# Optimization experiments

Measured on AMD Instinct MI355X. Metric: run time of the kernel, lower is better.

## Reference

```python
import jax, jax.numpy as jnp
import numpy as np

N, E, D, IN_DIM, EDGE_DIM, L = 50000, 800000, 128, 11, 4, 4
G, MID, SPEC = 500, 256, 300  # num graphs, decoder mid width, per-head spectrum dim
MSG_IN = 2 * D + EDGE_DIM + 1  # h_i, h_j, edge_attr, d2


def _lin_init(key, fan_in, shape):
    return jax.random.uniform(key, shape, jnp.float32, -1.0, 1.0) / np.sqrt(fan_in)


def setup_inputs() -> dict:
    key = jax.random.key(0)
    ks = iter(jax.random.split(key, 64))
    inp = {
        'x': jax.random.normal(next(ks), (N, IN_DIM), jnp.float32),
        'pos': jax.random.normal(next(ks), (N, 3), jnp.float32),
        'edge_attr': jax.random.normal(next(ks), (E, EDGE_DIM), jnp.float32),
        'edge_index': jax.random.randint(next(ks), (2, E), 0, N, jnp.int32),
        'batch': jnp.sort(jax.random.randint(next(ks), (N,), 0, G, jnp.int32)),
        # input projection
        'W_in': _lin_init(next(ks), IN_DIM, (IN_DIM, D)),
        'b_in': jnp.zeros((D,), jnp.float32),
        # per-layer message MLP: Linear(2D+de+1 -> D), ReLU, Linear(D -> D)
        'msg_W1': _lin_init(next(ks), MSG_IN, (L, MSG_IN, D)),
        'msg_b1': jnp.zeros((L, D), jnp.float32),
        'msg_W2': _lin_init(next(ks), D, (L, D, D)),
        'msg_b2': jnp.zeros((L, D), jnp.float32),
        # per-layer update MLP: Linear(2D -> D), ReLU, Linear(D -> D)
        'upd_W1': _lin_init(next(ks), 2 * D, (L, 2 * D, D)),
        'upd_b1': jnp.zeros((L, D), jnp.float32),
        'upd_W2': _lin_init(next(ks), D, (L, D, D)),
        'upd_b2': jnp.zeros((L, D), jnp.float32),
        # per-layer LayerNorm
        'ln_g': jnp.ones((L, D), jnp.float32),
        'ln_b': jnp.zeros((L, D), jnp.float32),
        # decoder heads stacked: index 0 = energy, 1 = intensity
        'dec_W1': _lin_init(next(ks), D, (2, D, MID)),
        'dec_b1': jnp.zeros((2, MID), jnp.float32),
        'dec_lng': jnp.ones((2, MID), jnp.float32),
        'dec_lnb': jnp.zeros((2, MID), jnp.float32),
        'dec_W2': _lin_init(next(ks), MID, (2, MID, MID)),
        'dec_b2': jnp.zeros((2, MID), jnp.float32),
        'dec_W3': _lin_init(next(ks), MID, (2, MID, SPEC)),
        'dec_b3': jnp.zeros((2, SPEC), jnp.float32),
    }
    return inp


def _ln(x, g, b, eps=1e-5):
    m = x.mean(-1, keepdims=True)
    v = ((x - m) ** 2).mean(-1, keepdims=True)
    return (x - m) * jax.lax.rsqrt(v + eps) * g + b


def _softplus_beta(x, beta):
    return jax.nn.softplus(beta * x) / beta


def reference(x, pos, edge_attr, edge_index, batch,
              W_in, b_in, msg_W1, msg_b1, msg_W2, msg_b2,
              upd_W1, upd_b1, upd_W2, upd_b2, ln_g, ln_b,
              dec_W1, dec_b1, dec_lng, dec_lnb, dec_W2, dec_b2, dec_W3, dec_b3):
    n = x.shape[0]
    src, dst = edge_index[0], edge_index[1]  # message flows j(src) -> i(dst)
    h = x @ W_in + b_in  # (n, d)
    rel = pos[dst] - pos[src]  # (e, 3)
    d2 = jnp.sum(rel * rel, axis=-1, keepdims=True)  # (e, 1), invariant squared distance
    for l in range(L):
        m_in = jnp.concatenate([h[dst], h[src], edge_attr, d2], axis=-1)  # (e, 2d+de+1)
        m = jax.nn.relu(m_in @ msg_W1[l] + msg_b1[l]) @ msg_W2[l] + msg_b2[l]  # (e, d)
        agg = jax.ops.segment_sum(m, dst, num_segments=n)  # (n, d) sum aggregation
        u_in = jnp.concatenate([h, agg], axis=-1)  # (n, 2d)
        h_upd = jax.nn.relu(u_in @ upd_W1[l] + upd_b1[l]) @ upd_W2[l] + upd_b2[l]
        h = _ln(h + h_upd, ln_g[l], ln_b[l])  # residual + LayerNorm
    # global mean pool per graph
    hs = jax.ops.segment_sum(h, batch, num_segments=G)
    cnt = jax.ops.segment_sum(jnp.ones((n,), h.dtype), batch, num_segments=G)
    hg = hs / jnp.clip(cnt, 1.0)[:, None]  # (G, d)

    def head(i):
        z = _softplus_beta(_ln(hg @ dec_W1[i] + dec_b1[i], dec_lng[i], dec_lnb[i]), 2.0)
        z = _softplus_beta(z @ dec_W2[i] + dec_b2[i], 2.0)  # dropout = identity (eval)
        return _softplus_beta(z @ dec_W3[i] + dec_b3[i], 1.0)

    eng, intensity = head(0), head(1)
    return jnp.concatenate([eng, intensity], axis=-1)  # (G, 2*SPEC)
```

## Files before the change

kernel.cpp:

```cpp
#include <hip/hip_runtime.h>
#include <cstdint>
#include <cstddef>

#define NND 50000
#define NE  800000
#define DD  128
#define NG  500
#define TT  64
#define NHB 50176

typedef __attribute__((ext_vector_type(8))) short short8v;
typedef __attribute__((ext_vector_type(4))) float float4v;

__device__ __forceinline__ short f2bf(float f) {
    unsigned u = __builtin_bit_cast(unsigned, f);
    unsigned r = (u + 0x7FFFu + ((u >> 16) & 1u)) >> 16;
    return (short)r;
}

__global__ __launch_bounds__(256) void inproj_kernel(
    const float* __restrict__ x, const float* __restrict__ W,
    const float* __restrict__ b, float* __restrict__ h)
{
    int t = blockIdx.x * 256 + threadIdx.x;
    int i = t >> 7, d = t & 127;
    if (i >= NND) return;
    const float* xr = x + (size_t)i * 11;
    float acc = b[d];
#pragma unroll
    for (int k = 0; k < 11; ++k) acc += xr[k] * W[k * DD + d];
    h[(size_t)i * DD + d] = acc;
}

__global__ __launch_bounds__(256) void hist_kernel(
    const int* __restrict__ dstI, int* __restrict__ hist)
{
    int e = blockIdx.x * 256 + threadIdx.x;
    if (e >= NE) return;
    atomicAdd(&hist[dstI[e]], 1);
}

__global__ __launch_bounds__(256) void scan1_kernel(
    int* __restrict__ hist, int* __restrict__ bsum)
{
    __shared__ int s[256];
    int tid = threadIdx.x;
    int i = blockIdx.x * 256 + tid;
    int v = hist[i];
    s[tid] = v; __syncthreads();
    for (int off = 1; off < 256; off <<= 1) {
        int tmp = (tid >= off) ? s[tid - off] : 0;
        __syncthreads();
        s[tid] += tmp;
        __syncthreads();
    }
    hist[i] = s[tid] - v;
    if (tid == 255) bsum[blockIdx.x] = s[255];
}

__global__ __launch_bounds__(256) void scan2_kernel(
    const int* __restrict__ bsum, int* __restrict__ bsumx)
{
    __shared__ int s[256];
    int tid = threadIdx.x;
    int v = (tid < 196) ? bsum[tid] : 0;
    s[tid] = v; __syncthreads();
    for (int off = 1; off < 256; off <<= 1) {
        int tmp = (tid >= off) ? s[tid - off] : 0;
        __syncthreads();
        s[tid] += tmp;
        __syncthreads();
    }
    if (tid < 196) bsumx[tid] = s[tid] - v;
}

__global__ __launch_bounds__(256) void scan3_kernel(
    int* __restrict__ hist, const int* __restrict__ bsumx)
{
    int i = blockIdx.x * 256 + threadIdx.x;
    hist[i] += bsumx[blockIdx.x];
}

__global__ __launch_bounds__(256) void scatter_kernel(
    const int* __restrict__ dstI, int* __restrict__ cursor, int* __restrict__ perm)
{
    int e = blockIdx.x * 256 + threadIdx.x;
    if (e >= NE) return;
    int pos = atomicAdd(&cursor[dstI[e]], 1);
    perm[pos] = e;
}

__global__ __launch_bounds__(256) void permapply_kernel(
    const int* __restrict__ perm, const int* __restrict__ srcI, const int* __restrict__ dstI,
    const float* __restrict__ ea,
    int* __restrict__ srcP, int* __restrict__ dstP, float* __restrict__ eaP)
{
    int i = blockIdx.x * 256 + threadIdx.x;
    if (i >= NE) return;
    int e = perm[i];
    srcP[i] = srcI[e];
    dstP[i] = dstI[e];
    ((float4*)eaP)[i] = ((const float4*)ea)[e];
}

__global__ __launch_bounds__(256) void d2p_kernel(
    const float* __restrict__ pos, const int* __restrict__ srcP,
    const int* __restrict__ dstP, float* __restrict__ d2)
{
    int e = blockIdx.x * 256 + threadIdx.x;
    if (e >= NE) return;
    int s = srcP[e], d = dstP[e];
    float dx = pos[d * 3 + 0] - pos[s * 3 + 0];
    float dy = pos[d * 3 + 1] - pos[s * 3 + 1];
    float dz = pos[d * 3 + 2] - pos[s * 3 + 2];
    d2[e] = dx * dx + dy * dy + dz * dz;
}

__global__ __launch_bounds__(256) void d2_kernel(
    const float* __restrict__ pos, const int* __restrict__ srcI,
    const int* __restrict__ dstI, float* __restrict__ d2)
{
    int e = blockIdx.x * 256 + threadIdx.x;
    if (e >= NE) return;
    int s = srcI[e], d = dstI[e];
    float dx = pos[d * 3 + 0] - pos[s * 3 + 0];
    float dy = pos[d * 3 + 1] - pos[s * 3 + 1];
    float dz = pos[d * 3 + 2] - pos[s * 3 + 2];
    d2[e] = dx * dx + dy * dy + dz * dz;
}

__global__ __launch_bounds__(256) void w2prep_kernel(
    const float* __restrict__ W2, short* __restrict__ W2t)
{
    int p = blockIdx.x * 256 + threadIdx.x;
    int n = p >> 7;
    int q = (p & 127) >> 3;
    int j = p & 7;
    int kg = q ^ (n & 7);
    W2t[p] = f2bf(W2[(kg * 8 + j) * DD + n]);
}

__global__ __launch_bounds__(256, 4) void proj_kernel(
    const float* __restrict__ h, const float* __restrict__ W1, float* __restrict__ P)
{
    __shared__ __align__(16) float A[32][TT];
    __shared__ __align__(16) float B[32][DD];
    int i0 = blockIdx.x * TT;
    int mat = blockIdx.y;
    const float* W = W1 + (size_t)mat * 128 * DD;
    float* out = P + (size_t)mat * NND * DD;
    int t = threadIdx.x;
    int tx = t & 15, ty = t >> 4;
    int e = t & 63, q = t >> 6;
    int node = i0 + e; if (node >= NND) node = NND - 1;
    const float* hrow = h + (size_t)node * DD;

    float acc[4][8];
#pragma unroll
    for (int i = 0; i < 4; ++i)
#pragma unroll
        for (int j = 0; j < 8; ++j) acc[i][j] = 0.0f;

    for (int c = 0; c < 4; ++c) {
        __syncthreads();
        float4 v0 = *(const float4*)(hrow + c * 32 + q * 8);
        float4 v1 = *(const float4*)(hrow + c * 32 + q * 8 + 4);
#pragma unroll
        for (int j = 0; j < 4; ++j) A[q * 8 + j][e]     = (&v0.x)[j];
#pragma unroll
        for (int j = 0; j < 4; ++j) A[q * 8 + 4 + j][e] = (&v1.x)[j];
        const float4* srcp = (const float4*)(W + (size_t)(c * 32) * DD);
        float4* dstp = (float4*)&B[0][0];
#pragma unroll
        for (int r = 0; r < 4; ++r) dstp[t + r * 256] = srcp[t + r * 256];
        __syncthreads();
#pragma unroll 4
        for (int k = 0; k < 32; ++k) {
            float4 a  = *(const float4*)&A[k][tx * 4];
            float4 b0 = *(const float4*)&B[k][ty * 8];
            float4 b1 = *(const float4*)&B[k][ty * 8 + 4];
            float av[4] = {a.x, a.y, a.z, a.w};
            float bv[8] = {b0.x, b0.y, b0.z, b0.w, b1.x, b1.y, b1.z, b1.w};
#pragma unroll
            for (int i = 0; i < 4; ++i)
#pragma unroll
                for (int j = 0; j < 8; ++j) acc[i][j] += av[i] * bv[j];
        }
    }
#pragma unroll
    for (int i = 0; i < 4; ++i) {
        int r = i0 + tx * 4 + i;
        if (r < NND) {
            float4 o0 = {acc[i][0], acc[i][1], acc[i][2], acc[i][3]};
            float4 o1 = {acc[i][4], acc[i][5], acc[i][6], acc[i][7]};
            *(float4*)(out + (size_t)r * DD + ty * 8)     = o0;
            *(float4*)(out + (size_t)r * DD + ty * 8 + 4) = o1;
        }
    }
}

__global__ __launch_bounds__(256, 3) void msgm_kernel(
    const float* __restrict__ P, const int* __restrict__ srcP, const int* __restrict__ dstP,
    const float* __restrict__ eaP, const float* __restrict__ d2,
    const float* __restrict__ W1tail, const float* __restrict__ b1,
    const short* __restrict__ W2t, const float* __restrict__ b2,
    float* __restrict__ agg)
{
    __shared__ __align__(16) short Tld[64 * 128];
    __shared__ __align__(16) short W2ld[128 * 128];
    int t = threadIdx.x;
    int e0 = blockIdx.x * TT;
    int tx = t & 15, ty = t >> 4;

    {
        const short8v* g = (const short8v*)W2t;
        short8v* l = (short8v*)W2ld;
#pragma unroll
        for (int p = 0; p < 8; ++p) l[t + p * 256] = g[t + p * 256];
    }

    float wc[5][8];
#pragma unroll
    for (int qf = 0; qf < 5; ++qf) {
        float4 a0 = *(const float4*)(W1tail + qf * DD + ty * 8);
        float4 a1 = *(const float4*)(W1tail + qf * DD + ty * 8 + 4);
        wc[qf][0] = a0.x; wc[qf][1] = a0.y; wc[qf][2] = a0.z; wc[qf][3] = a0.w;
        wc[qf][4] = a1.x; wc[qf][5] = a1.y; wc[qf][6] = a1.z; wc[qf][7] = a1.w;
    }

    float4 b1a = *(const float4*)(b1 + ty * 8);
    float4 b1b = *(const float4*)(b1 + ty * 8 + 4);
    float b1v[8] = {b1a.x, b1a.y, b1a.z, b1a.w, b1b.x, b1b.y, b1b.z, b1b.w};

    const float* Pd = P;
    const float* Ps = P + (size_t)NND * DD;

    int4 dv4 = *(const int4*)(dstP + e0 + tx * 4);
    int4 sv4 = *(const int4*)(srcP + e0 + tx * 4);
    int dcache[4] = {dv4.x, dv4.y, dv4.z, dv4.w};
    int scache[4] = {sv4.x, sv4.y, sv4.z, sv4.w};

#pragma unroll
    for (int i = 0; i < 4; ++i) {
        int e = tx * 4 + i;
        const float* pd = Pd + (size_t)dcache[i] * DD + ty * 8;
        const float* ps = Ps + (size_t)scache[i] * DD + ty * 8;
        float4 p0 = *(const float4*)pd;
        float4 p1 = *(const float4*)(pd + 4);
        float4 q0 = *(const float4*)ps;
        float4 q1 = *(const float4*)(ps + 4);
        float tv[8] = {p0.x + q0.x, p0.y + q0.y, p0.z + q0.z, p0.w + q0.w,
                       p1.x + q1.x, p1.y + q1.y, p1.z + q1.z, p1.w + q1.w};
#pragma unroll
        for (int j = 0; j < 8; ++j) tv[j] += b1v[j];
        float4 av = ((const float4*)eaP)[e0 + e];
        float ev[5] = {av.x, av.y, av.z, av.w, d2[e0 + e]};
#pragma unroll
        for (int qf = 0; qf < 5; ++qf) {
            float xx = ev[qf];
#pragma unroll
            for (int j = 0; j < 8; ++j) tv[j] += xx * wc[qf][j];
        }
        short8v pk;
#pragma unroll
        for (int j = 0; j < 8; ++j) pk[j] = f2bf(fmaxf(tv[j], 0.0f));
        int colg = ty ^ (e & 7);
        *(short8v*)&Tld[e * 128 + colg * 8] = pk;
    }

    __syncthreads();

    int lane = t & 63, w = t >> 6;
    int lg = lane >> 4;
    int m  = w * 16 + (lane & 15);
    float4v acc[8];
#pragma unroll
    for (int i = 0; i < 8; ++i) acc[i] = (float4v){0.f, 0.f, 0.f, 0.f};

#pragma unroll
    for (int ks = 0; ks < 4; ++ks) {
        int kg = ks * 4 + lg;
        short8v afrag = *(const short8v*)&Tld[m * 128 + ((kg ^ (m & 7)) << 3)];
#pragma unroll
        for (int nt = 0; nt < 8; ++nt) {
            int n = nt * 16 + (lane & 15);
            short8v bfrag = *(const short8v*)&W2ld[n * 128 + ((kg ^ (n & 7)) << 3)];
            acc[nt] = __builtin_amdgcn_mfma_f32_16x16x32_bf16(afrag, bfrag, acc[nt], 0, 0, 0);
        }
    }

    int base_e = e0 + w * 16 + (lg << 2);
    int4 dq = *(const int4*)(dstP + base_e);
    int drow[4] = {dq.x, dq.y, dq.z, dq.w};
    float b2c[8];
#pragma unroll
    for (int nt = 0; nt < 8; ++nt) b2c[nt] = b2[nt * 16 + (lane & 15)];

    float sum[8];
    int cur = drow[0];
#pragma unroll
    for (int nt = 0; nt < 8; ++nt) sum[nt] = acc[nt][0] + b2c[nt];
#pragma unroll
    for (int r = 1; r < 4; ++r) {
        if (drow[r] == cur) {
#pragma unroll
            for (int nt = 0; nt < 8; ++nt) sum[nt] += acc[nt][r] + b2c[nt];
        } else {
            float* ag = agg + (size_t)cur * DD + (lane & 15);
#pragma unroll
            for (int nt = 0; nt < 8; ++nt) unsafeAtomicAdd(ag + nt * 16, sum[nt]);
            cur = drow[r];
#pragma unroll
            for (int nt = 0; nt < 8; ++nt) sum[nt] = acc[nt][r] + b2c[nt];
        }
    }
    float* ag = agg + (size_t)cur * DD + (lane & 15);
#pragma unroll
    for (int nt = 0; nt < 8; ++nt) unsafeAtomicAdd(ag + nt * 16, sum[nt]);
}

__global__ __launch_bounds__(256, 3) void msgf_kernel(
    const float* __restrict__ P, const int* __restrict__ srcI, const int* __restrict__ dstI,
    const float* __restrict__ ea, const float* __restrict__ d2,
    const float* __restrict__ W1tail, const float* __restrict__ b1,
    const float* __restrict__ W2, const float* __restrict__ b2,
    float* __restrict__ agg)
{
    __shared__ __align__(16) float T[DD][TT];
    __shared__ __align__(16) float B[32][DD];
    __shared__ __align__(16) float Wc[5][DD];
    int t = threadIdx.x;
    int e0 = blockIdx.x * TT;
    int tx = t & 15, ty = t >> 4;

    if (t < 160) ((float4*)&Wc[0][0])[t] = ((const float4*)W1tail)[t];
    __syncthreads();

    float4 b1a = *(const float4*)(b1 + ty * 8);
    float4 b1b = *(const float4*)(b1 + ty * 8 + 4);
    float b1v[8] = {b1a.x, b1a.y, b1a.z, b1a.w, b1b.x, b1b.y, b1b.z, b1b.w};

    const float* Pd = P;
    const float* Ps = P + (size_t)NND * DD;
    int dcache[4];
#pragma unroll
    for (int i = 0; i < 4; ++i) {
        int e  = tx * 4 + i;
        int ds = dstI[e0 + e];
        int sr = srcI[e0 + e];
        dcache[i] = ds;
        const float* pd = Pd + (size_t)ds * DD + ty * 8;
        const float* ps = Ps + (size_t)sr * DD + ty * 8;
        float4 p0 = *(const float4*)pd;
        float4 p1 = *(const float4*)(pd + 4);
        float4 q0 = *(const float4*)ps;
        float4 q1 = *(const float4*)(ps + 4);
        float tv[8] = {p0.x + q0.x, p0.y + q0.y, p0.z + q0.z, p0.w + q0.w,
                       p1.x + q1.x, p1.y + q1.y, p1.z + q1.z, p1.w + q1.w};
#pragma unroll
        for (int j = 0; j < 8; ++j) tv[j] += b1v[j];
        float4 av = ((const float4*)ea)[e0 + e];
        float ev[5] = {av.x, av.y, av.z, av.w, d2[e0 + e]};
#pragma unroll
        for (int qf = 0; qf < 5; ++qf) {
            float xx = ev[qf];
#pragma unroll
            for (int j = 0; j < 8; ++j) tv[j] += xx * Wc[qf][ty * 8 + j];
        }
#pragma unroll
        for (int j = 0; j < 8; ++j) T[ty * 8 + j][e] = fmaxf(tv[j], 0.0f);
    }

    float4 b2a = *(const float4*)(b2 + ty * 8);
    float4 b2b = *(const float4*)(b2 + ty * 8 + 4);
    float acc[4][8];
#pragma unroll
    for (int i = 0; i < 4; ++i) {
        acc[i][0] = b2a.x; acc[i][1] = b2a.y; acc[i][2] = b2a.z; acc[i][3] = b2a.w;
        acc[i][4] = b2b.x; acc[i][5] = b2b.y; acc[i][6] = b2b.z; acc[i][7] = b2b.w;
    }

    for (int c = 0; c < 4; ++c) {
        __syncthreads();
        const float4* srcp = (const float4*)(W2 + (size_t)(c * 32) * DD);
        float4* dstp = (float4*)&B[0][0];
#pragma unroll
        for (int r = 0; r < 4; ++r) dstp[t + r * 256] = srcp[t + r * 256];
        __syncthreads();
#pragma unroll 4
        for (int k = 0; k < 32; ++k) {
            float4 a  = *(const float4*)&T[c * 32 + k][tx * 4];
            float4 b0 = *(const float4*)&B[k][ty * 8];
            float4 b1f = *(const float4*)&B[k][ty * 8 + 4];
            float av[4] = {a.x, a.y, a.z, a.w};
            float bv[8] = {b0.x, b0.y, b0.z, b0.w, b1f.x, b1f.y, b1f.z, b1f.w};
#pragma unroll
            for (int i = 0; i < 4; ++i)
#pragma unroll
                for (int j = 0; j < 8; ++j) acc[i][j] += av[i] * bv[j];
        }
    }

#pragma unroll
    for (int i = 0; i < 4; ++i) {
        float* ag = agg + (size_t)dcache[i] * DD + ty * 8;
#pragma unroll
        for (int j = 0; j < 8; ++j) unsafeAtomicAdd(ag + j, acc[i][j]);
    }
}

__global__ __launch_bounds__(256, 2) void upd_kernel(
    float* __restrict__ h, const float* __restrict__ agg,
    const float* __restrict__ W1, const float* __restrict__ b1,
    const float* __restrict__ W2, const float* __restrict__ b2,
    const float* __restrict__ lng, const float* __restrict__ lnb)
{
    __shared__ __align__(16) float A[32][TT];
    __shared__ __align__(16) float T[DD][TT];
    __shared__ __align__(16) float B[32][DD];
    int t = threadIdx.x;
    int i0 = blockIdx.x * TT;
    int tx = t & 15, ty = t >> 4;
    int e = t & 63, q = t >> 6;
    int node = i0 + e; int nclamp = (node < NND) ? node : (NND - 1);

    float4 b1a = *(const float4*)(b1 + ty * 8);
    float4 b1b = *(const float4*)(b1 + ty * 8 + 4);
    float acc[4][8];
#pragma unroll
    for (int i = 0; i < 4; ++i) {
        acc[i][0] = b1a.x; acc[i][1] = b1a.y; acc[i][2] = b1a.z; acc[i][3] = b1a.w;
        acc[i][4] = b1b.x; acc[i][5] = b1b.y; acc[i][6] = b1b.z; acc[i][7] = b1b.w;
    }

    for (int c = 0; c < 8; ++c) {
        __syncthreads();
        const float* row = ((c < 4) ? (h + (size_t)nclamp * DD + c * 32)
                                    : (agg + (size_t)nclamp * DD + (c - 4) * 32));
        float4 v0 = *(const float4*)(row + q * 8);
        float4 v1 = *(const float4*)(row + q * 8 + 4);
#pragma unroll
        for (int j = 0; j < 4; ++j) A[q * 8 + j][e]     = (&v0.x)[j];
#pragma unroll
        for (int j = 0; j < 4; ++j) A[q * 8 + 4 + j][e] = (&v1.x)[j];
        const float4* srcp = (const float4*)(W1 + (size_t)(c * 32) * DD);
        float4* dstp = (float4*)&B[0][0];
#pragma unroll
        for (int r = 0; r < 4; ++r) dstp[t + r * 256] = srcp[t + r * 256];
        __syncthreads();
#pragma unroll 4
        for (int k = 0; k < 32; ++k) {
            float4 a  = *(const float4*)&A[k][tx * 4];
            float4 b0 = *(const float4*)&B[k][ty * 8];
            float4 b1f = *(const float4*)&B[k][ty * 8 + 4];
            float av[4] = {a.x, a.y, a.z, a.w};
            float bv[8] = {b0.x, b0.y, b0.z, b0.w, b1f.x, b1f.y, b1f.z, b1f.w};
#pragma unroll
            for (int i = 0; i < 4; ++i)
#pragma unroll
                for (int j = 0; j < 8; ++j) acc[i][j] += av[i] * bv[j];
        }
    }

#pragma unroll
    for (int i = 0; i < 4; ++i)
#pragma unroll
        for (int j = 0; j < 8; ++j) T[ty * 8 + j][tx * 4 + i] = fmaxf(acc[i][j], 0.0f);

    float4 b2a = *(const float4*)(b2 + ty * 8);
    float4 b2b = *(const float4*)(b2 + ty * 8 + 4);
#pragma unroll
    for (int i = 0; i < 4; ++i) {
        acc[i][0] = b2a.x; acc[i][1] = b2a.y; acc[i][2] = b2a.z; acc[i][3] = b2a.w;
        acc[i][4] = b2b.x; acc[i][5] = b2b.y; acc[i][6] = b2b.z; acc[i][7] = b2b.w;
    }
    for (int c = 0; c < 4; ++c) {
        __syncthreads();
        const float4* srcp = (const float4*)(W2 + (size_t)(c * 32) * DD);
        float4* dstp = (float4*)&B[0][0];
#pragma unroll
        for (int r = 0; r < 4; ++r) dstp[t + r * 256] = srcp[t + r * 256];
        __syncthreads();
#pragma unroll 4
        for (int k = 0; k < 32; ++k) {
            float4 a  = *(const float4*)&T[c * 32 + k][tx * 4];
            float4 b0 = *(const float4*)&B[k][ty * 8];
            float4 b1f = *(const float4*)&B[k][ty * 8 + 4];
            float av[4] = {a.x, a.y, a.z, a.w};
            float bv[8] = {b0.x, b0.y, b0.z, b0.w, b1f.x, b1f.y, b1f.z, b1f.w};
#pragma unroll
            for (int i = 0; i < 4; ++i)
#pragma unroll
                for (int j = 0; j < 8; ++j) acc[i][j] += av[i] * bv[j];
        }
    }

    __syncthreads();
#pragma unroll
    for (int i = 0; i < 4; ++i)
#pragma unroll
        for (int j = 0; j < 8; ++j) T[ty * 8 + j][tx * 4 + i] = acc[i][j];
    __syncthreads();

    if (t < TT) {
        int nd = i0 + t;
        if (nd < NND) {
            float* hrow = h + (size_t)nd * DD;
            float sum = 0.0f;
            for (int o = 0; o < DD; ++o) sum += T[o][t] + hrow[o];
            float mean = sum * (1.0f / DD);
            float var = 0.0f;
            for (int o = 0; o < DD; ++o) {
                float xv = T[o][t] + hrow[o] - mean;
                var += xv * xv;
            }
            var *= (1.0f / DD);
            float inv = 1.0f / sqrtf(var + 1e-5f);
            for (int o = 0; o < DD; ++o) {
                float xv = T[o][t] + hrow[o];
                hrow[o] = (xv - mean) * inv * lng[o] + lnb[o];
            }
        }
    }
}

__global__ __launch_bounds__(256) void cnt_kernel(
    const int* __restrict__ batch, float* __restrict__ cnt)
{
    int i = blockIdx.x * 256 + threadIdx.x;
    if (i >= NND) return;
    unsafeAtomicAdd(&cnt[batch[i]], 1.0f);
}

__global__ __launch_bounds__(256) void pool_kernel(
    const float* __restrict__ h, const int* __restrict__ batch, float* __restrict__ hs)
{
    int t = blockIdx.x * 256 + threadIdx.x;
    int i = t >> 7, d = t & 127;
    if (i >= NND) return;
    unsafeAtomicAdd(&hs[batch[i] * DD + d], h[(size_t)i * DD + d]);
}

__device__ __forceinline__ float softplus_stable(float y) {
    return fmaxf(y, 0.0f) + log1pf(expf(-fabsf(y)));
}

__global__ __launch_bounds__(256) void dec_kernel(
    const float* __restrict__ hs, const float* __restrict__ cnt,
    const float* __restrict__ W1, const float* __restrict__ b1,
    const float* __restrict__ lng, const float* __restrict__ lnb,
    const float* __restrict__ W2, const float* __restrict__ b2,
    const float* __restrict__ W3, const float* __restrict__ b3,
    float* __restrict__ out)
{
    int g  = blockIdx.x >> 1;
    int hd = blockIdx.x & 1;
    int t  = threadIdx.x;
    __shared__ float hg[DD];
    __shared__ float sA[256];
    __shared__ float red[256];

    if (t < DD) {
        float c = fmaxf(cnt[g], 1.0f);
        hg[t] = hs[g * DD + t] / c;
    }
    __syncthreads();

    const float* w1 = W1 + hd * DD * 256;
    float acc = b1[hd * 256 + t];
#pragma unroll 8
    for (int k = 0; k < DD; ++k) acc += hg[k] * w1[k * 256 + t];

    red[t] = acc; __syncthreads();
    for (int s = 128; s > 0; s >>= 1) { if (t < s) red[t] += red[t + s]; __syncthreads(); }
    float mean = red[0] * (1.0f / 256.0f);
    __syncthreads();
    float dv = acc - mean;
    red[t] = dv * dv; __syncthreads();
    for (int s = 128; s > 0; s >>= 1) { if (t < s) red[t] += red[t + s]; __syncthreads(); }
    float var = red[0] * (1.0f / 256.0f);
    float inv = 1.0f / sqrtf(var + 1e-5f);
    float z1 = dv * inv * lng[hd * 256 + t] + lnb[hd * 256 + t];
    z1 = softplus_stable(2.0f * z1) * 0.5f;
    __syncthreads();
    sA[t] = z1; __syncthreads();

    const float* w2 = W2 + hd * 256 * 256;
    float acc2 = b2[hd * 256 + t];
#pragma unroll 8
    for (int k = 0; k < 256; ++k) acc2 += sA[k] * w2[k * 256 + t];
    float z2 = softplus_stable(2.0f * acc2) * 0.5f;
    __syncthreads();
    sA[t] = z2; __syncthreads();

    const float* w3 = W3 + hd * 256 * 300;
    for (int s = t; s < 300; s += 256) {
        float acc3 = b3[hd * 300 + s];
#pragma unroll 8
        for (int k = 0; k < 256; ++k) acc3 += sA[k] * w3[k * 300 + s];
        out[g * 600 + hd * 300 + s] = softplus_stable(acc3);
    }
}

extern "C" void kernel_launch(void* const* d_in, const int* in_sizes, int n_in,
                              void* d_out, int out_size, void* d_ws, size_t ws_size,
                              hipStream_t stream)
{
    const float* x     = (const float*)d_in[0];
    const float* pos   = (const float*)d_in[1];
    const float* eattr = (const float*)d_in[2];
    const int*   eidx  = (const int*)d_in[3];
    const int*   batch = (const int*)d_in[4];
    const float* W_in  = (const float*)d_in[5];
    const float* b_in  = (const float*)d_in[6];
    const float* msgW1 = (const float*)d_in[7];
    const float* msgb1 = (const float*)d_in[8];
    const float* msgW2 = (const float*)d_in[9];
    const float* msgb2 = (const float*)d_in[10];
    const float* updW1 = (const float*)d_in[11];
    const float* updb1 = (const float*)d_in[12];
    const float* updW2 = (const float*)d_in[13];
    const float* updb2 = (const float*)d_in[14];
    const float* lng   = (const float*)d_in[15];
    const float* lnb   = (const float*)d_in[16];
    const float* dW1   = (const float*)d_in[17];
    const float* db1   = (const float*)d_in[18];
    const float* dlng  = (const float*)d_in[19];
    const float* dlnb  = (const float*)d_in[20];
    const float* dW2   = (const float*)d_in[21];
    const float* db2   = (const float*)d_in[22];
    const float* dW3   = (const float*)d_in[23];
    const float* db3   = (const float*)d_in[24];

    float* ws  = (float*)d_ws;
    float* h    = ws;
    float* agg  = ws + 6400000;
    float* d2   = ws + 12800000;
    float* hsg  = ws + 13600000;
    float* cnt  = ws + 13664000;
    short* W2t  = (short*)(ws + 13666000);
    float* P    = ws + 13700000;
    int*   perm = (int*)(ws + 26500000);
    int*   srcP = (int*)(ws + 27300000);
    int*   dstP = (int*)(ws + 28100000);
    float* eaP  = ws + 28900000;
    int*   hist = (int*)(ws + 32100000);
    int*   bsum = (int*)(ws + 32150176);
    int*   bsumx= (int*)(ws + 32150432);

    const size_t need_sorted   = (size_t)32150688 * 4;
    const size_t need_factored = (size_t)(13700000 + 2 * NND * DD) * 4;
    const bool sorted   = (ws_size >= need_sorted);
    const bool factored = (ws_size >= need_factored);

    const int* srcI = eidx;
    const int* dstI = eidx + NE;

    inproj_kernel<<<25000, 256, 0, stream>>>(x, W_in, b_in, h);

    if (sorted) {
        hipMemsetAsync(hist, 0, (size_t)(NHB + 512) * 4, stream);
        hist_kernel<<<3125, 256, 0, stream>>>(dstI, hist);
        scan1_kernel<<<196, 256, 0, stream>>>(hist, bsum);
        scan2_kernel<<<1, 256, 0, stream>>>(bsum, bsumx);
        scan3_kernel<<<196, 256, 0, stream>>>(hist, bsumx);
        scatter_kernel<<<3125, 256, 0, stream>>>(dstI, hist, perm);
        permapply_kernel<<<3125, 256, 0, stream>>>(perm, srcI, dstI, eattr, srcP, dstP, eaP);
        d2p_kernel<<<3125, 256, 0, stream>>>(pos, srcP, dstP, d2);
    } else {
        d2_kernel<<<3125, 256, 0, stream>>>(pos, srcI, dstI, d2);
    }

    const int nblk_nodes = (NND + TT - 1) / TT;
    const int nblk_edges = NE / TT;

    for (int l = 0; l < 4; ++l) {
        const float* W1l = msgW1 + (size_t)l * 261 * 128;
        hipMemsetAsync(agg, 0, 6400000 * sizeof(float), stream);
        if (sorted) {
            w2prep_kernel<<<64, 256, 0, stream>>>(msgW2 + (size_t)l * 128 * 128, W2t);
            proj_kernel<<<dim3(nblk_nodes, 2), 256, 0, stream>>>(h, W1l, P);
            msgm_kernel<<<nblk_edges, 256, 0, stream>>>(P, srcP, dstP, eaP, d2,
                W1l + 256 * 128, msgb1 + l * 128, W2t, msgb2 + l * 128, agg);
        } else if (factored) {
            proj_kernel<<<dim3(nblk_nodes, 2), 256, 0, stream>>>(h, W1l, P);
            msgf_kernel<<<nblk_edges, 256, 0, stream>>>(P, srcI, dstI, eattr, d2,
                W1l + 256 * 128, msgb1 + l * 128,
                msgW2 + (size_t)l * 128 * 128, msgb2 + l * 128, agg);
        }
        upd_kernel<<<nblk_nodes, 256, 0, stream>>>(h, agg,
            updW1 + (size_t)l * 256 * 128, updb1 + l * 128,
            updW2 + (size_t)l * 128 * 128, updb2 + l * 128,
            lng + l * 128, lnb + l * 128);
    }

    hipMemsetAsync(hsg, 0, 64500 * sizeof(float), stream);
    cnt_kernel<<<196, 256, 0, stream>>>(batch, cnt);
    pool_kernel<<<25000, 256, 0, stream>>>(h, batch, hsg);
    dec_kernel<<<1000, 256, 0, stream>>>(hsg, cnt, dW1, db1, dlng, dlnb,
                                         dW2, db2, dW3, db3, (float*)d_out);
}
```

Baseline: 2.234 ms.

## Move node projection and update MLP to bf16 MFMA with prepacked weights

Per layer, all weight matrices (msg W2, both halves of upd W1, upd W2, and both halves of msg W1) are converted to swizzled bf16 in one prep kernel. The node projection and update MLP with LayerNorm now run on MFMA 16x16x32 bf16 instructions instead of fp32 FMA loops. The shared-memory swizzle is extended to XOR the row's bits 3-5 as well, to reduce LDS bank conflicts. The fallback path is rebuilt to an unfactored fp32 message kernel, and the change adds bf16 rounding to the h and agg inputs of the update MLP.

```diff
diff --git a/kernel.cpp b/kernel.cpp
--- a/kernel.cpp
+++ b/kernel.cpp
@@ -11,6 +11,8 @@
 
 typedef __attribute__((ext_vector_type(8))) short short8v;
 typedef __attribute__((ext_vector_type(4))) float float4v;
+
+#define SWZA(row, g) ((g) ^ ((row) & 7) ^ (((row) >> 3) & 7))
 
 __device__ __forceinline__ short f2bf(float f) {
     unsigned u = __builtin_bit_cast(unsigned, f);
@@ -129,72 +131,96 @@
     d2[e] = dx * dx + dy * dy + dz * dz;
 }
 
-__global__ __launch_bounds__(256) void w2prep_kernel(
-    const float* __restrict__ W2, short* __restrict__ W2t)
+__global__ __launch_bounds__(256) void wprep_kernel(
+    const float* __restrict__ msgW2, const float* __restrict__ updW1,
+    const float* __restrict__ updW2, const float* __restrict__ msgW1,
+    short* __restrict__ out)
 {
     int p = blockIdx.x * 256 + threadIdx.x;
-    int n = p >> 7;
-    int q = (p & 127) >> 3;
-    int j = p & 7;
-    int kg = q ^ (n & 7);
-    W2t[p] = f2bf(W2[(kg * 8 + j) * DD + n]);
-}
-
-__global__ __launch_bounds__(256, 4) void proj_kernel(
-    const float* __restrict__ h, const float* __restrict__ W1, float* __restrict__ P)
-{
-    __shared__ __align__(16) float A[32][TT];
-    __shared__ __align__(16) float B[32][DD];
+    int chunk = p >> 14;
+    int idx = p & 16383;
+    int n = idx >> 7;
+    int q = (idx & 127) >> 3;
+    int j = idx & 7;
+    int k = (q ^ (n & 7)) * 8 + j;
+    const float* src;
+    if      (chunk == 0) src = msgW2;
+    else if (chunk == 1) src = updW1;
+    else if (chunk == 2) src = updW1 + 128 * DD;
+    else if (chunk == 3) src = updW2;
+    else if (chunk == 4) src = msgW1;
+    else                 src = msgW1 + 128 * DD;
+    out[p] = f2bf(src[k * DD + n]);
+}
+
+__global__ __launch_bounds__(256, 3) void projm_kernel(
+    const float* __restrict__ h, const short* __restrict__ Wa, const short* __restrict__ Wb,
+    float* __restrict__ P)
+{
+    __shared__ __align__(16) short A[64 * 128];
+    __shared__ __align__(16) short W[128 * 128];
+    int t = threadIdx.x;
     int i0 = blockIdx.x * TT;
-    int mat = blockIdx.y;
-    const float* W = W1 + (size_t)mat * 128 * DD;
-    float* out = P + (size_t)mat * NND * DD;
-    int t = threadIdx.x;
-    int tx = t & 15, ty = t >> 4;
-    int e = t & 63, q = t >> 6;
-    int node = i0 + e; if (node >= NND) node = NND - 1;
-    const float* hrow = h + (size_t)node * DD;
-
-    float acc[4][8];
-#pragma unroll
-    for (int i = 0; i < 4; ++i)
-#pragma unroll
-        for (int j = 0; j < 8; ++j) acc[i][j] = 0.0f;
-
-    for (int c = 0; c < 4; ++c) {
-        __syncthreads();
-        float4 v0 = *(const float4*)(hrow + c * 32 + q * 8);
-        float4 v1 = *(const float4*)(hrow + c * 32 + q * 8 + 4);
-#pragma unroll
-        for (int j = 0; j < 4; ++j) A[q * 8 + j][e]     = (&v0.x)[j];
-#pragma unroll
-        for (int j = 0; j < 4; ++j) A[q * 8 + 4 + j][e] = (&v1.x)[j];
-        const float4* srcp = (const float4*)(W + (size_t)(c * 32) * DD);
-        float4* dstp = (float4*)&B[0][0];
-#pragma unroll
-        for (int r = 0; r < 4; ++r) dstp[t + r * 256] = srcp[t + r * 256];
-        __syncthreads();
-#pragma unroll 4
-        for (int k = 0; k < 32; ++k) {
-            float4 a  = *(const float4*)&A[k][tx * 4];
-            float4 b0 = *(const float4*)&B[k][ty * 8];
-            float4 b1 = *(const float4*)&B[k][ty * 8 + 4];
-            float av[4] = {a.x, a.y, a.z, a.w};
-            float bv[8] = {b0.x, b0.y, b0.z, b0.w, b1.x, b1.y, b1.z, b1.w};
-#pragma unroll
-            for (int i = 0; i < 4; ++i)
-#pragma unroll
-                for (int j = 0; j < 8; ++j) acc[i][j] += av[i] * bv[j];
-        }
-    }
-#pragma unroll
-    for (int i = 0; i < 4; ++i) {
-        int r = i0 + tx * 4 + i;
-        if (r < NND) {
-            float4 o0 = {acc[i][0], acc[i][1], acc[i][2], acc[i][3]};
-            float4 o1 = {acc[i][4], acc[i][5], acc[i][6], acc[i][7]};
-            *(float4*)(out + (size_t)r * DD + ty * 8)     = o0;
-            *(float4*)(out + (size_t)r * DD + ty * 8 + 4) = o1;
+
+    {
+        int e = t >> 2;
+        int node = i0 + e; if (node >= NND) node = NND - 1;
+        const float* hr = h + (size_t)node * DD;
+#pragma unroll
+        for (int j = 0; j < 4; ++j) {
+            int g = (t & 3) * 4 + j;
+            float4 v0 = *(const float4*)(hr + g * 8);
+            float4 v1 = *(const float4*)(hr + g * 8 + 4);
+            short8v pk;
+            pk[0]=f2bf(v0.x); pk[1]=f2bf(v0.y); pk[2]=f2bf(v0.z); pk[3]=f2bf(v0.w);
+            pk[4]=f2bf(v1.x); pk[5]=f2bf(v1.y); pk[6]=f2bf(v1.z); pk[7]=f2bf(v1.w);
+            *(short8v*)&A[e * 128 + SWZA(e, g) * 8] = pk;
+        }
+    }
+    {
+        const short8v* g = (const short8v*)Wa;
+        short8v* l = (short8v*)W;
+#pragma unroll
+        for (int p = 0; p < 8; ++p) l[t + p * 256] = g[t + p * 256];
+    }
+    __syncthreads();
+
+    int lane = t & 63, w = t >> 6;
+    int c = lane & 15, lg = lane >> 4;
+    int m = w * 16 + c;
+
+    for (int mat = 0; mat < 2; ++mat) {
+        float4v acc[8];
+#pragma unroll
+        for (int i = 0; i < 8; ++i) acc[i] = (float4v){0.f, 0.f, 0.f, 0.f};
+#pragma unroll
+        for (int ks = 0; ks < 4; ++ks) {
+            int kg = ks * 4 + lg;
+            short8v afrag = *(const short8v*)&A[m * 128 + SWZA(m, kg) * 8];
+#pragma unroll
+            for (int nt = 0; nt < 8; ++nt) {
+                int n = nt * 16 + c;
+                short8v bfrag = *(const short8v*)&W[n * 128 + ((kg ^ (n & 7)) << 3)];
+                acc[nt] = __builtin_amdgcn_mfma_f32_16x16x32_bf16(afrag, bfrag, acc[nt], 0, 0, 0);
+            }
+        }
+        float* out = P + (size_t)mat * NND * DD;
+#pragma unroll
+        for (int reg = 0; reg < 4; ++reg) {
+            int node = i0 + w * 16 + lg * 4 + reg;
+            if (node < NND) {
+#pragma unroll
+                for (int nt = 0; nt < 8; ++nt)
+                    out[(size_t)node * DD + nt * 16 + c] = acc[nt][reg];
+            }
+        }
+        if (mat == 0) {
+            __syncthreads();
+            const short8v* g = (const short8v*)Wb;
+            short8v* l = (short8v*)W;
+#pragma unroll
+            for (int p = 0; p < 8; ++p) l[t + p * 256] = g[t + p * 256];
+            __syncthreads();
         }
     }
 }
@@ -264,8 +290,7 @@
         short8v pk;
 #pragma unroll
         for (int j = 0; j < 8; ++j) pk[j] = f2bf(fmaxf(tv[j], 0.0f));
-        int colg = ty ^ (e & 7);
-        *(short8v*)&Tld[e * 128 + colg * 8] = pk;
+        *(short8v*)&Tld[e * 128 + SWZA(e, ty) * 8] = pk;
     }
 
     __syncthreads();
@@ -280,7 +305,7 @@
 #pragma unroll
     for (int ks = 0; ks < 4; ++ks) {
         int kg = ks * 4 + lg;
-        short8v afrag = *(const short8v*)&Tld[m * 128 + ((kg ^ (m & 7)) << 3)];
+        short8v afrag = *(const short8v*)&Tld[m * 128 + SWZA(m, kg) * 8];
 #pragma unroll
         for (int nt = 0; nt < 8; ++nt) {
             int n = nt * 16 + (lane & 15);
@@ -319,77 +344,234 @@
     for (int nt = 0; nt < 8; ++nt) unsafeAtomicAdd(ag + nt * 16, sum[nt]);
 }
 
-__global__ __launch_bounds__(256, 3) void msgf_kernel(
-    const float* __restrict__ P, const int* __restrict__ srcI, const int* __restrict__ dstI,
+__global__ __launch_bounds__(256, 3) void updm_kernel(
+    float* __restrict__ h, const float* __restrict__ agg,
+    const short* __restrict__ W1a, const short* __restrict__ W1b, const short* __restrict__ W2s,
+    const float* __restrict__ b1, const float* __restrict__ b2,
+    const float* __restrict__ lng, const float* __restrict__ lnb)
+{
+    __shared__ __align__(16) short A[64 * 128];
+    __shared__ __align__(16) short W[128 * 128];
+    int t = threadIdx.x;
+    int i0 = blockIdx.x * TT;
+    int lane = t & 63, w = t >> 6;
+    int c = lane & 15, lg = lane >> 4;
+    int m = w * 16 + c;
+
+    {
+        int e = t >> 2;
+        int node = i0 + e; if (node >= NND) node = NND - 1;
+        const float* hr = h + (size_t)node * DD;
+#pragma unroll
+        for (int j = 0; j < 4; ++j) {
+            int g = (t & 3) * 4 + j;
+            float4 v0 = *(const float4*)(hr + g * 8);
+            float4 v1 = *(const float4*)(hr + g * 8 + 4);
+            short8v pk;
+            pk[0]=f2bf(v0.x); pk[1]=f2bf(v0.y); pk[2]=f2bf(v0.z); pk[3]=f2bf(v0.w);
+            pk[4]=f2bf(v1.x); pk[5]=f2bf(v1.y); pk[6]=f2bf(v1.z); pk[7]=f2bf(v1.w);
+            *(short8v*)&A[e * 128 + SWZA(e, g) * 8] = pk;
+        }
+        const short8v* gg = (const short8v*)W1a;
+        short8v* l = (short8v*)W;
+#pragma unroll
+        for (int p = 0; p < 8; ++p) l[t + p * 256] = gg[t + p * 256];
+    }
+    __syncthreads();
+
+    float4v acc[8];
+#pragma unroll
+    for (int i = 0; i < 8; ++i) acc[i] = (float4v){0.f, 0.f, 0.f, 0.f};
+
+#pragma unroll
+    for (int ks = 0; ks < 4; ++ks) {
+        int kg = ks * 4 + lg;
+        short8v afrag = *(const short8v*)&A[m * 128 + SWZA(m, kg) * 8];
+#pragma unroll
+        for (int nt = 0; nt < 8; ++nt) {
+            int n = nt * 16 + c;
+            short8v bfrag = *(const short8v*)&W[n * 128 + ((kg ^ (n & 7)) << 3)];
+            acc[nt] = __builtin_amdgcn_mfma_f32_16x16x32_bf16(afrag, bfrag, acc[nt], 0, 0, 0);
+        }
+    }
+    __syncthreads();
+
+    {
+        int e = t >> 2;
+        int node = i0 + e; if (node >= NND) node = NND - 1;
+        const float* ar = agg + (size_t)node * DD;
+#pragma unroll
+        for (int j = 0; j < 4; ++j) {
+            int g = (t & 3) * 4 + j;
+            float4 v0 = *(const float4*)(ar + g * 8);
+            float4 v1 = *(const float4*)(ar + g * 8 + 4);
+            short8v pk;
+            pk[0]=f2bf(v0.x); pk[1]=f2bf(v0.y); pk[2]=f2bf(v0.z); pk[3]=f2bf(v0.w);
+            pk[4]=f2bf(v1.x); pk[5]=f2bf(v1.y); pk[6]=f2bf(v1.z); pk[7]=f2bf(v1.w);
+            *(short8v*)&A[e * 128 + SWZA(e, g) * 8] = pk;
+        }
+        const short8v* gg = (const short8v*)W1b;
+        short8v* l = (short8v*)W;
+#pragma unroll
+        for (int p = 0; p < 8; ++p) l[t + p * 256] = gg[t + p * 256];
+    }
+    __syncthreads();
+
+#pragma unroll
+    for (int ks = 0; ks < 4; ++ks) {
+        int kg = ks * 4 + lg;
+        short8v afrag = *(const short8v*)&A[m * 128 + SWZA(m, kg) * 8];
+#pragma unroll
+        for (int nt = 0; nt < 8; ++nt) {
+            int n = nt * 16 + c;
+            short8v bfrag = *(const short8v*)&W[n * 128 + ((kg ^ (n & 7)) << 3)];
+            acc[nt] = __builtin_amdgcn_mfma_f32_16x16x32_bf16(afrag, bfrag, acc[nt], 0, 0, 0);
+        }
+    }
+    __syncthreads();
+
+    {
+        float b1c[8];
+#pragma unroll
+        for (int nt = 0; nt < 8; ++nt) b1c[nt] = b1[nt * 16 + c];
+#pragma unroll
+        for (int reg = 0; reg < 4; ++reg) {
+            int rowT = w * 16 + lg * 4 + reg;
+#pragma unroll
+            for (int nt = 0; nt < 8; ++nt) {
+                int col = nt * 16 + c;
+                int colg = col >> 3;
+                float v = fmaxf(acc[nt][reg] + b1c[nt], 0.0f);
+                A[rowT * 128 + SWZA(rowT, colg) * 8 + (col & 7)] = f2bf(v);
+            }
+        }
+        const short8v* gg = (const short8v*)W2s;
+        short8v* l = (short8v*)W;
+#pragma unroll
+        for (int p = 0; p < 8; ++p) l[t + p * 256] = gg[t + p * 256];
+    }
+    __syncthreads();
+
+#pragma unroll
+    for (int i = 0; i < 8; ++i) acc[i] = (float4v){0.f, 0.f, 0.f, 0.f};
+#pragma unroll
+    for (int ks = 0; ks < 4; ++ks) {
+        int kg = ks * 4 + lg;
+        short8v afrag = *(const short8v*)&A[m * 128 + SWZA(m, kg) * 8];
+#pragma unroll
+        for (int nt = 0; nt < 8; ++nt) {
+            int n = nt * 16 + c;
+            short8v bfrag = *(const short8v*)&W[n * 128 + ((kg ^ (n & 7)) << 3)];
+            acc[nt] = __builtin_amdgcn_mfma_f32_16x16x32_bf16(afrag, bfrag, acc[nt], 0, 0, 0);
+        }
+    }
+
+    float b2c[8], lngc[8], lnbc[8];
+#pragma unroll
+    for (int nt = 0; nt < 8; ++nt) {
+        b2c[nt]  = b2[nt * 16 + c];
+        lngc[nt] = lng[nt * 16 + c];
+        lnbc[nt] = lnb[nt * 16 + c];
+    }
+    float xx[8][4];
+#pragma unroll
+    for (int reg = 0; reg < 4; ++reg) {
+        int node = i0 + w * 16 + lg * 4 + reg;
+        int nclamp = (node < NND) ? node : (NND - 1);
+        const float* hr = h + (size_t)nclamp * DD;
+#pragma unroll
+        for (int nt = 0; nt < 8; ++nt)
+            xx[nt][reg] = acc[nt][reg] + b2c[nt] + hr[nt * 16 + c];
+    }
+    float s[4] = {0.f, 0.f, 0.f, 0.f};
+#pragma unroll
+    for (int reg = 0; reg < 4; ++reg)
+#pragma unroll
+        for (int nt = 0; nt < 8; ++nt) s[reg] += xx[nt][reg];
+#pragma unroll
+    for (int msk = 1; msk < 16; msk <<= 1)
+#pragma unroll
+        for (int reg = 0; reg < 4; ++reg) s[reg] += __shfl_xor(s[reg], msk, 64);
+    float mean[4];
+#pragma unroll
+    for (int reg = 0; reg < 4; ++reg) mean[reg] = s[reg] * (1.0f / DD);
+    float v[4] = {0.f, 0.f, 0.f, 0.f};
+#pragma unroll
+    for (int reg = 0; reg < 4; ++reg)
+#pragma unroll
+        for (int nt = 0; nt < 8; ++nt) {
+            float dv = xx[nt][reg] - mean[reg];
+            v[reg] += dv * dv;
+        }
+#pragma unroll
+    for (int msk = 1; msk < 16; msk <<= 1)
+#pragma unroll
+        for (int reg = 0; reg < 4; ++reg) v[reg] += __shfl_xor(v[reg], msk, 64);
+#pragma unroll
+    for (int reg = 0; reg < 4; ++reg) {
+        int node = i0 + w * 16 + lg * 4 + reg;
+        if (node < NND) {
+            float inv = 1.0f / sqrtf(v[reg] * (1.0f / DD) + 1e-5f);
+            float* hw = h + (size_t)node * DD;
+#pragma unroll
+            for (int nt = 0; nt < 8; ++nt)
+                hw[nt * 16 + c] = (xx[nt][reg] - mean[reg]) * inv * lngc[nt] + lnbc[nt];
+        }
+    }
+}
+
+__global__ __launch_bounds__(256, 2) void msgu_kernel(
+    const float* __restrict__ h, const int* __restrict__ srcI, const int* __restrict__ dstI,
     const float* __restrict__ ea, const float* __restrict__ d2,
-    const float* __restrict__ W1tail, const float* __restrict__ b1,
+    const float* __restrict__ W1, const float* __restrict__ b1,
     const float* __restrict__ W2, const float* __restrict__ b2,
     float* __restrict__ agg)
 {
+    __shared__ __align__(16) float A[32][TT];
     __shared__ __align__(16) float T[DD][TT];
     __shared__ __align__(16) float B[32][DD];
-    __shared__ __align__(16) float Wc[5][DD];
     int t = threadIdx.x;
     int e0 = blockIdx.x * TT;
     int tx = t & 15, ty = t >> 4;
-
-    if (t < 160) ((float4*)&Wc[0][0])[t] = ((const float4*)W1tail)[t];
-    __syncthreads();
+    int e = t & 63, q = t >> 6;
+    int dn = dstI[e0 + e], sn = srcI[e0 + e];
 
     float4 b1a = *(const float4*)(b1 + ty * 8);
     float4 b1b = *(const float4*)(b1 + ty * 8 + 4);
-    float b1v[8] = {b1a.x, b1a.y, b1a.z, b1a.w, b1b.x, b1b.y, b1b.z, b1b.w};
-
-    const float* Pd = P;
-    const float* Ps = P + (size_t)NND * DD;
-    int dcache[4];
+    float acc[4][8];
 #pragma unroll
     for (int i = 0; i < 4; ++i) {
-        int e  = tx * 4 + i;
-        int ds = dstI[e0 + e];
-        int sr = srcI[e0 + e];
-        dcache[i] = ds;
-        const float* pd = Pd + (size_t)ds * DD + ty * 8;
-        const float* ps = Ps + (size_t)sr * DD + ty * 8;
-        float4 p0 = *(const float4*)pd;
-        float4 p1 = *(const float4*)(pd + 4);
-        float4 q0 = *(const float4*)ps;
-        float4 q1 = *(const float4*)(ps + 4);
-        float tv[8] = {p0.x + q0.x, p0.y + q0.y, p0.z + q0.z, p0.w + q0.w,
-                       p1.x + q1.x, p1.y + q1.y, p1.z + q1.z, p1.w + q1.w};
-#pragma unroll
-        for (int j = 0; j < 8; ++j) tv[j] += b1v[j];
-        float4 av = ((const float4*)ea)[e0 + e];
-        float ev[5] = {av.x, av.y, av.z, av.w, d2[e0 + e]};
-#pragma unroll
-        for (int qf = 0; qf < 5; ++qf) {
-            float xx = ev[qf];
-#pragma unroll
-            for (int j = 0; j < 8; ++j) tv[j] += xx * Wc[qf][ty * 8 + j];
-        }
-#pragma unroll
-        for (int j = 0; j < 8; ++j) T[ty * 8 + j][e] = fmaxf(tv[j], 0.0f);
-    }
-
-    float4 b2a = *(const float4*)(b2 + ty * 8);
-    float4 b2b = *(const float4*)(b2 + ty * 8 + 4);
-    float acc[4][8];
-#pragma unroll
-    for (int i = 0; i < 4; ++i) {
-        acc[i][0] = b2a.x; acc[i][1] = b2a.y; acc[i][2] = b2a.z; acc[i][3] = b2a.w;
-        acc[i][4] = b2b.x; acc[i][5] = b2b.y; acc[i][6] = b2b.z; acc[i][7] = b2b.w;
-    }
-
-    for (int c = 0; c < 4; ++c) {
-        __syncthreads();
-        const float4* srcp = (const float4*)(W2 + (size_t)(c * 32) * DD);
+        acc[i][0] = b1a.x; acc[i][1] = b1a.y; acc[i][2] = b1a.z; acc[i][3] = b1a.w;
+        acc[i][4] = b1b.x; acc[i][5] = b1b.y; acc[i][6] = b1b.z; acc[i][7] = b1b.w;
+    }
+
+    for (int cc = 0; cc < 9; ++cc) {
+        int kmax = (cc == 8) ? 5 : 32;
+        __syncthreads();
+        if (cc < 8) {
+            const float* row = h + (size_t)((cc < 4) ? dn : sn) * DD + (cc & 3) * 32;
+            float4 v0 = *(const float4*)(row + q * 8);
+            float4 v1 = *(const float4*)(row + q * 8 + 4);
+#pragma unroll
+            for (int j = 0; j < 4; ++j) A[q * 8 + j][e]     = (&v0.x)[j];
+#pragma unroll
+            for (int j = 0; j < 4; ++j) A[q * 8 + 4 + j][e] = (&v1.x)[j];
+        } else if (t < TT) {
+            float4 av = ((const float4*)ea)[e0 + t];
+            A[0][t] = av.x; A[1][t] = av.y; A[2][t] = av.z; A[3][t] = av.w;
+            A[4][t] = d2[e0 + t];
+        }
+        const float4* srcp = (const float4*)(W1 + (size_t)(cc * 32) * DD);
         float4* dstp = (float4*)&B[0][0];
-#pragma unroll
-        for (int r = 0; r < 4; ++r) dstp[t + r * 256] = srcp[t + r * 256];
-        __syncthreads();
-#pragma unroll 4
-        for (int k = 0; k < 32; ++k) {
-            float4 a  = *(const float4*)&T[c * 32 + k][tx * 4];
+        if (cc < 8) {
+#pragma unroll
+            for (int r = 0; r < 4; ++r) dstp[t + r * 256] = srcp[t + r * 256];
+        } else if (t < 160) {
+            dstp[t] = srcp[t];
+        }
+        __syncthreads();
+        for (int k = 0; k < kmax; ++k) {
+            float4 a  = *(const float4*)&A[k][tx * 4];
             float4 b0 = *(const float4*)&B[k][ty * 8];
             float4 b1f = *(const float4*)&B[k][ty * 8 + 4];
             float av[4] = {a.x, a.y, a.z, a.w};
@@ -402,14 +584,47 @@
     }
 
 #pragma unroll
+    for (int i = 0; i < 4; ++i)
+#pragma unroll
+        for (int j = 0; j < 8; ++j) T[ty * 8 + j][tx * 4 + i] = fmaxf(acc[i][j], 0.0f);
+
+    float4 b2a = *(const float4*)(b2 + ty * 8);
+    float4 b2b = *(const float4*)(b2 + ty * 8 + 4);
+#pragma unroll
     for (int i = 0; i < 4; ++i) {
-        float* ag = agg + (size_t)dcache[i] * DD + ty * 8;
+        acc[i][0] = b2a.x; acc[i][1] = b2a.y; acc[i][2] = b2a.z; acc[i][3] = b2a.w;
+        acc[i][4] = b2b.x; acc[i][5] = b2b.y; acc[i][6] = b2b.z; acc[i][7] = b2b.w;
+    }
+    for (int cc = 0; cc < 4; ++cc) {
+        __syncthreads();
+        const float4* srcp = (const float4*)(W2 + (size_t)(cc * 32) * DD);
+        float4* dstp = (float4*)&B[0][0];
+#pragma unroll
+        for (int r = 0; r < 4; ++r) dstp[t + r * 256] = srcp[t + r * 256];
+        __syncthreads();
+#pragma unroll 4
+        for (int k = 0; k < 32; ++k) {
+            float4 a  = *(const float4*)&T[cc * 32 + k][tx * 4];
+            float4 b0 = *(const float4*)&B[k][ty * 8];
+            float4 b1f = *(const float4*)&B[k][ty * 8 + 4];
+            float av[4] = {a.x, a.y, a.z, a.w};
+            float bv[8] = {b0.x, b0.y, b0.z, b0.w, b1f.x, b1f.y, b1f.z, b1f.w};
+#pragma unroll
+            for (int i = 0; i < 4; ++i)
+#pragma unroll
+                for (int j = 0; j < 8; ++j) acc[i][j] += av[i] * bv[j];
+        }
+    }
+#pragma unroll
+    for (int i = 0; i < 4; ++i) {
+        int d = dstI[e0 + tx * 4 + i];
+        float* ag = agg + (size_t)d * DD + ty * 8;
 #pragma unroll
         for (int j = 0; j < 8; ++j) unsafeAtomicAdd(ag + j, acc[i][j]);
     }
 }
 
-__global__ __launch_bounds__(256, 2) void upd_kernel(
+__global__ __launch_bounds__(256, 2) void updf_kernel(
     float* __restrict__ h, const float* __restrict__ agg,
     const float* __restrict__ W1, const float* __restrict__ b1,
     const float* __restrict__ W2, const float* __restrict__ b2,
@@ -433,17 +648,17 @@
         acc[i][4] = b1b.x; acc[i][5] = b1b.y; acc[i][6] = b1b.z; acc[i][7] = b1b.w;
     }
 
-    for (int c = 0; c < 8; ++c) {
-        __syncthreads();
-        const float* row = ((c < 4) ? (h + (size_t)nclamp * DD + c * 32)
-                                    : (agg + (size_t)nclamp * DD + (c - 4) * 32));
+    for (int cc = 0; cc < 8; ++cc) {
+        __syncthreads();
+        const float* row = ((cc < 4) ? (h + (size_t)nclamp * DD + cc * 32)
+                                     : (agg + (size_t)nclamp * DD + (cc - 4) * 32));
         float4 v0 = *(const float4*)(row + q * 8);
         float4 v1 = *(const float4*)(row + q * 8 + 4);
 #pragma unroll
         for (int j = 0; j < 4; ++j) A[q * 8 + j][e]     = (&v0.x)[j];
 #pragma unroll
         for (int j = 0; j < 4; ++j) A[q * 8 + 4 + j][e] = (&v1.x)[j];
-        const float4* srcp = (const float4*)(W1 + (size_t)(c * 32) * DD);
+        const float4* srcp = (const float4*)(W1 + (size_t)(cc * 32) * DD);
         float4* dstp = (float4*)&B[0][0];
 #pragma unroll
         for (int r = 0; r < 4; ++r) dstp[t + r * 256] = srcp[t + r * 256];
@@ -474,16 +689,16 @@
         acc[i][0] = b2a.x; acc[i][1] = b2a.y; acc[i][2] = b2a.z; acc[i][3] = b2a.w;
         acc[i][4] = b2b.x; acc[i][5] = b2b.y; acc[i][6] = b2b.z; acc[i][7] = b2b.w;
     }
-    for (int c = 0; c < 4; ++c) {
-        __syncthreads();
-        const float4* srcp = (const float4*)(W2 + (size_t)(c * 32) * DD);
+    for (int cc = 0; cc < 4; ++cc) {
+        __syncthreads();
+        const float4* srcp = (const float4*)(W2 + (size_t)(cc * 32) * DD);
         float4* dstp = (float4*)&B[0][0];
 #pragma unroll
         for (int r = 0; r < 4; ++r) dstp[t + r * 256] = srcp[t + r * 256];
         __syncthreads();
 #pragma unroll 4
         for (int k = 0; k < 32; ++k) {
-            float4 a  = *(const float4*)&T[c * 32 + k][tx * 4];
+            float4 a  = *(const float4*)&T[cc * 32 + k][tx * 4];
             float4 b0 = *(const float4*)&B[k][ty * 8];
             float4 b1f = *(const float4*)&B[k][ty * 8 + 4];
             float av[4] = {a.x, a.y, a.z, a.w};
@@ -561,8 +776,8 @@
     __shared__ float red[256];
 
     if (t < DD) {
-        float c = fmaxf(cnt[g], 1.0f);
-        hg[t] = hs[g * DD + t] / c;
+        float cct = fmaxf(cnt[g], 1.0f);
+        hg[t] = hs[g * DD + t] / cct;
     }
     __syncthreads();
 
@@ -638,7 +853,6 @@
     float* d2   = ws + 12800000;
     float* hsg  = ws + 13600000;
     float* cnt  = ws + 13664000;
-    short* W2t  = (short*)(ws + 13666000);
     float* P    = ws + 13700000;
     int*   perm = (int*)(ws + 26500000);
     int*   srcP = (int*)(ws + 27300000);
@@ -647,11 +861,10 @@
     int*   hist = (int*)(ws + 32100000);
     int*   bsum = (int*)(ws + 32150176);
     int*   bsumx= (int*)(ws + 32150432);
-
-    const size_t need_sorted   = (size_t)32150688 * 4;
-    const size_t need_factored = (size_t)(13700000 + 2 * NND * DD) * 4;
-    const bool sorted   = (ws_size >= need_sorted);
-    const bool factored = (ws_size >= need_factored);
+    short* WP   = (short*)(ws + 32150688);
+
+    const size_t need_sorted = (size_t)(32150688 + 49152) * 4;
+    const bool sorted = (ws_size >= need_sorted);
 
     const int* srcI = eidx;
     const int* dstI = eidx + NE;
@@ -678,20 +891,24 @@
         const float* W1l = msgW1 + (size_t)l * 261 * 128;
         hipMemsetAsync(agg, 0, 6400000 * sizeof(float), stream);
         if (sorted) {
-            w2prep_kernel<<<64, 256, 0, stream>>>(msgW2 + (size_t)l * 128 * 128, W2t);
-            proj_kernel<<<dim3(nblk_nodes, 2), 256, 0, stream>>>(h, W1l, P);
+            wprep_kernel<<<384, 256, 0, stream>>>(
+                msgW2 + (size_t)l * 128 * 128, updW1 + (size_t)l * 256 * 128,
+                updW2 + (size_t)l * 128 * 128, W1l, WP);
+            projm_kernel<<<nblk_nodes, 256, 0, stream>>>(h, WP + 4 * 16384, WP + 5 * 16384, P);
             msgm_kernel<<<nblk_edges, 256, 0, stream>>>(P, srcP, dstP, eaP, d2,
-                W1l + 256 * 128, msgb1 + l * 128, W2t, msgb2 + l * 128, agg);
-        } else if (factored) {
-            proj_kernel<<<dim3(nblk_nodes, 2), 256, 0, stream>>>(h, W1l, P);
-            msgf_kernel<<<nblk_edges, 256, 0, stream>>>(P, srcI, dstI, eattr, d2,
-                W1l + 256 * 128, msgb1 + l * 128,
+                W1l + 256 * 128, msgb1 + l * 128, WP, msgb2 + l * 128, agg);
+            updm_kernel<<<nblk_nodes, 256, 0, stream>>>(h, agg,
+                WP + 1 * 16384, WP + 2 * 16384, WP + 3 * 16384,
+                updb1 + l * 128, updb2 + l * 128, lng + l * 128, lnb + l * 128);
+        } else {
+            msgu_kernel<<<nblk_edges, 256, 0, stream>>>(h, srcI, dstI, eattr, d2,
+                W1l, msgb1 + l * 128,
                 msgW2 + (size_t)l * 128 * 128, msgb2 + l * 128, agg);
-        }
-        upd_kernel<<<nblk_nodes, 256, 0, stream>>>(h, agg,
-            updW1 + (size_t)l * 256 * 128, updb1 + l * 128,
-            updW2 + (size_t)l * 128 * 128, updb2 + l * 128,
-            lng + l * 128, lnb + l * 128);
+            updf_kernel<<<nblk_nodes, 256, 0, stream>>>(h, agg,
+                updW1 + (size_t)l * 256 * 128, updb1 + l * 128,
+                updW2 + (size_t)l * 128 * 128, updb2 + l * 128,
+                lng + l * 128, lnb + l * 128);
+        }
     }
 
     hipMemsetAsync(hsg, 0, 64500 * sizeof(float), stream);
```

Measured after the change: 1.849 ms. 1.21x faster.
